# Kernel tuning notes

Measured on AMD Instinct MI355X. Metric: run time of the kernel, lower is better.

The kernel has to match this reference:

```python
import jax, jax.numpy as jnp
import numpy as np

FP4_E2M1_VALUES = jnp.array([0.0, 0.5, 1.0, 1.5, 2.0, 3.0, 4.0, 6.0,
                             -0.0, -0.5, -1.0, -1.5, -2.0, -3.0, -4.0, -6.0],
                            dtype=jnp.float32)

OUT_F, IN_F, BS = 4096, 4096, 16


def setup_inputs() -> dict:
    key = jax.random.key(0)
    k1, k2, k3, k4 = jax.random.split(key, 4)
    x = jax.random.normal(k1, (4, 2048, IN_F), dtype=jnp.float32)
    weight_indices = jax.random.randint(k2, (OUT_F, IN_F // BS, BS), 0, 16, dtype=jnp.int32)
    weight_scales = jax.random.uniform(k3, (OUT_F, IN_F // BS), dtype=jnp.float32)
    bias = jax.random.normal(k4, (OUT_F,), dtype=jnp.float32)
    return {"x": x, "weight_indices": weight_indices,
            "weight_scales": weight_scales, "bias": bias}


def reference(x, weight_indices, weight_scales, bias):
    # Dequantize: gather FP4 values per index, scale per block of 16.
    idx = jnp.clip(weight_indices, 0, 15)              # [O, NB, BS]
    vals = FP4_E2M1_VALUES[idx]                        # [O, NB, BS]
    weight = (vals * weight_scales[:, :, None]).reshape(OUT_F, IN_F)
    # F.linear: y = x @ W^T + b
    return jnp.einsum('bsi,oi->bso', x, weight) + bias
```

## Files before the change

### kernel.cpp

```cpp
#include <hip/hip_runtime.h>
#include <hip/hip_bf16.h>

static constexpr int M_TOT = 8192;
static constexpr int N_TOT = 4096;
static constexpr int K_TOT = 4096;

static constexpr int BM = 256, BN = 256, BK = 32;
static constexpr int NT = K_TOT / BK;
static constexpr int GTHREADS = 512;
static constexpr int BUF_BYTES = 32768;
static constexpr int LDS_BYTES = 4 * BUF_BYTES;

typedef __bf16 bf16x8 __attribute__((ext_vector_type(8)));
typedef float f32x4 __attribute__((ext_vector_type(4)));
typedef unsigned short u16x8 __attribute__((ext_vector_type(8)));

__device__ __forceinline__ unsigned short f2bf(float f) {
  return __builtin_bit_cast(unsigned short, (__bf16)f);
}

__device__ __forceinline__ float fp4_decode(int idx) {
  unsigned u = (unsigned)idx & 15u;
  unsigned sgn = (u >> 3) << 31;
  unsigned mag = u & 7u;
  unsigned e = mag >> 1, m = mag & 1u;
  unsigned bits = (e == 0u) ? (m ? 0x3F000000u : 0u)
                            : (((126u + e) << 23) | (m << 22));
  return __uint_as_float(bits | sgn);
}

__device__ __forceinline__ void glds16(const void* g, void* l) {
  __builtin_amdgcn_global_load_lds(
      (__attribute__((address_space(1))) void*)g,
      (__attribute__((address_space(3))) void*)l, 16, 0, 0);
}

__global__ __launch_bounds__(256) void dequant_w_kernel(
    const int* __restrict__ idx, const float* __restrict__ scales,
    unsigned short* __restrict__ W) {
  const int t = blockIdx.x * 256 + threadIdx.x;
  const int4 v = reinterpret_cast<const int4*>(idx)[t];
  const float s = scales[t >> 2];
  ushort4 o;
  o.x = f2bf(fp4_decode(v.x) * s);
  o.y = f2bf(fp4_decode(v.y) * s);
  o.z = f2bf(fp4_decode(v.z) * s);
  o.w = f2bf(fp4_decode(v.w) * s);
  reinterpret_cast<ushort4*>(W)[t] = o;
}

__global__ __launch_bounds__(256) void convert_x_kernel(
    const float* __restrict__ x, unsigned short* __restrict__ A) {
  const int t = blockIdx.x * 256 + threadIdx.x;
  const float4* xp = reinterpret_cast<const float4*>(x);
  const float4 a = xp[2 * t], b = xp[2 * t + 1];
  u16x8 o;
  o[0] = f2bf(a.x); o[1] = f2bf(a.y); o[2] = f2bf(a.z); o[3] = f2bf(a.w);
  o[4] = f2bf(b.x); o[5] = f2bf(b.y); o[6] = f2bf(b.z); o[7] = f2bf(b.w);
  reinterpret_cast<u16x8*>(A)[t] = o;
}

__global__ __launch_bounds__(GTHREADS, 1) void gemm256(
    const unsigned short* __restrict__ A, const unsigned short* __restrict__ B,
    const float* __restrict__ bias, float* __restrict__ out) {
  extern __shared__ char smem[];

  const int t = threadIdx.x;
  const int lane = t & 63, wid = t >> 6;
  const int wr = wid >> 2;
  const int wc = wid & 3;
  const int ln = lane & 15;
  const int kc = lane >> 4;

  const int bid = blockIdx.x;
  const int bmi = (bid & 7) * 4 + ((bid >> 3) & 3);
  const int bni = bid >> 5;
  const int bm0 = bmi * BM, bn0 = bni * BN;

  const int row_s = t >> 2;
  const int kcd = (t & 3) ^ ((t >> 3) & 3);
  const unsigned short* gA = A + (size_t)(bm0 + row_s) * K_TOT + kcd * 8;
  const unsigned short* gB = B + (size_t)(bn0 + row_s) * K_TOT + kcd * 8;
  char* ldsA = smem + t * 16;
  char* ldsB = smem + 16384 + t * 16;

  const int swz = (kc ^ ((ln >> 1) & 3)) * 16;
  const int base_a = (wr * 128 + ln) * 64 + swz;
  const int base_b = 16384 + (wc * 64 + ln) * 64 + swz;

  f32x4 acc[8][4];
#pragma unroll
  for (int i = 0; i < 8; ++i)
#pragma unroll
    for (int j = 0; j < 4; ++j) acc[i][j] = f32x4{0.f, 0.f, 0.f, 0.f};

  bf16x8 afA[4], afB[4], bfE[4], bfO[4];

#define STAGE_A(kt, bufi) do {                                          \
    const unsigned short* s_ = gA + (size_t)(kt) * BK;                  \
    glds16(s_, ldsA + (bufi) * BUF_BYTES);                              \
    glds16(s_ + (size_t)128 * K_TOT, ldsA + (bufi) * BUF_BYTES + 8192); \
  } while (0)
#define STAGE_B(kt, bufi) do {                                          \
    const unsigned short* s_ = gB + (size_t)(kt) * BK;                  \
    glds16(s_, ldsB + (bufi) * BUF_BYTES);                              \
    glds16(s_ + (size_t)128 * K_TOT, ldsB + (bufi) * BUF_BYTES + 8192); \
  } while (0)

#define READ_AF(dst, bufi, mb) do {                                     \
    const char* p_ = smem + (bufi) * BUF_BYTES + base_a + (mb) * 1024;  \
    dst[0] = *(const bf16x8*)(p_);                                      \
    dst[1] = *(const bf16x8*)(p_ + 1024);                               \
    dst[2] = *(const bf16x8*)(p_ + 2048);                               \
    dst[3] = *(const bf16x8*)(p_ + 3072);                               \
  } while (0)
#define READ_BF(dst, bufi) do {                                         \
    const char* p_ = smem + (bufi) * BUF_BYTES + base_b;                \
    dst[0] = *(const bf16x8*)(p_);                                      \
    dst[1] = *(const bf16x8*)(p_ + 1024);                               \
    dst[2] = *(const bf16x8*)(p_ + 2048);                               \
    dst[3] = *(const bf16x8*)(p_ + 3072);                               \
  } while (0)

#define MFMA16(afs, bfs, mb) do {                                       \
    __builtin_amdgcn_s_setprio(1);                                      \
    _Pragma("unroll")                                                   \
    for (int m_ = 0; m_ < 4; ++m_)                                      \
      _Pragma("unroll")                                                 \
      for (int n_ = 0; n_ < 4; ++n_)                                    \
        acc[(mb) + m_][n_] = __builtin_amdgcn_mfma_f32_16x16x32_bf16(   \
            afs[m_], bfs[n_], acc[(mb) + m_][n_], 0, 0, 0);             \
    __builtin_amdgcn_s_setprio(0);                                      \
  } while (0)

#define VM(n) asm volatile("s_waitcnt vmcnt(" #n ")" ::: "memory")
#define BAR __builtin_amdgcn_s_barrier()

#define PH_A(tt, rb, sb, bfc) do { \
    READ_AF(afB, rb, 4);           \
    STAGE_A((tt) + 3, sb);         \
    MFMA16(afA, bfc, 0);           \
    VM(6); BAR;                    \
  } while (0)
#define PH_B(tt, rbn, sb, bfc, bfn) do { \
    READ_AF(afA, rbn, 0);                \
    READ_BF(bfn, rbn);                   \
    STAGE_B((tt) + 3, sb);               \
    MFMA16(afB, bfc, 4);                 \
    BAR;                                 \
  } while (0)

  STAGE_A(0, 0); STAGE_B(0, 0);
  asm volatile("" ::: "memory");
  STAGE_A(1, 1); STAGE_B(1, 1);
  asm volatile("" ::: "memory");
  STAGE_A(2, 2); STAGE_B(2, 2);
  VM(8);
  BAR;
  READ_AF(afA, 0, 0);
  READ_BF(bfE, 0);

#pragma unroll 1
  for (int tt = 0; tt < NT - 4; tt += 4) {
    PH_A(tt + 0, 0, 3, bfE);
    PH_B(tt + 0, 1, 3, bfE, bfO);
    PH_A(tt + 1, 1, 0, bfO);
    PH_B(tt + 1, 2, 0, bfO, bfE);
    PH_A(tt + 2, 2, 1, bfE);
    PH_B(tt + 2, 3, 1, bfE, bfO);
    PH_A(tt + 3, 3, 2, bfO);
    PH_B(tt + 3, 0, 2, bfO, bfE);
  }

  READ_AF(afB, 0, 4); STAGE_A(127, 3); MFMA16(afA, bfE, 0); VM(6); BAR;
  READ_AF(afA, 1, 0); READ_BF(bfO, 1); STAGE_B(127, 3); MFMA16(afB, bfE, 4); BAR;
  READ_AF(afB, 1, 4); MFMA16(afA, bfO, 0); VM(4); BAR;
  READ_AF(afA, 2, 0); READ_BF(bfE, 2); MFMA16(afB, bfO, 4); BAR;
  READ_AF(afB, 2, 4); MFMA16(afA, bfE, 0); VM(0); BAR;
  READ_AF(afA, 3, 0); READ_BF(bfO, 3); MFMA16(afB, bfE, 4); BAR;
  READ_AF(afB, 3, 4); MFMA16(afA, bfO, 0);
  MFMA16(afB, bfO, 4);

  const int orow0 = bm0 + wr * 128 + (lane >> 4) * 4;
  const int ocol0 = bn0 + wc * 64 + ln;
  float bj[4];
#pragma unroll
  for (int n = 0; n < 4; ++n) bj[n] = bias[ocol0 + n * 16];
#pragma unroll
  for (int mi = 0; mi < 8; ++mi)
#pragma unroll
    for (int n = 0; n < 4; ++n)
#pragma unroll
      for (int q = 0; q < 4; ++q)
        out[(size_t)(orow0 + mi * 16 + q) * N_TOT + ocol0 + n * 16] =
            acc[mi][n][q] + bj[n];
}

extern "C" void kernel_launch(void* const* d_in, const int* in_sizes, int n_in,
                              void* d_out, int out_size, void* d_ws, size_t ws_size,
                              hipStream_t stream) {
  const float* x = (const float*)d_in[0];
  const int* widx = (const int*)d_in[1];
  const float* wsc = (const float*)d_in[2];
  const float* bias = (const float*)d_in[3];
  float* out = (float*)d_out;

  unsigned short* Abf = (unsigned short*)d_ws;
  unsigned short* Wbf = (unsigned short*)((char*)d_ws + (size_t)M_TOT * K_TOT * 2);

  convert_x_kernel<<<dim3((M_TOT * (size_t)K_TOT / 8) / 256), dim3(256), 0, stream>>>(x, Abf);
  dequant_w_kernel<<<dim3((N_TOT * (size_t)K_TOT / 4) / 256), dim3(256), 0, stream>>>(widx, wsc, Wbf);

  (void)hipFuncSetAttribute((const void*)gemm256,
                            hipFuncAttributeMaxDynamicSharedMemorySize, LDS_BYTES);
  gemm256<<<dim3((M_TOT / BM) * (N_TOT / BN)), dim3(GTHREADS), LDS_BYTES, stream>>>(
      Abf, Wbf, bias, out);
}
```

Measured before the change: 279.2 us.

## Switch GEMM inner product to 32x32x16 bf16 MFMA tiles

```diff
diff --git a/kernel.cpp b/kernel.cpp
--- a/kernel.cpp
+++ b/kernel.cpp
@@ -12,7 +12,7 @@
 static constexpr int LDS_BYTES = 4 * BUF_BYTES;
 
 typedef __bf16 bf16x8 __attribute__((ext_vector_type(8)));
-typedef float f32x4 __attribute__((ext_vector_type(4)));
+typedef float f32x16 __attribute__((ext_vector_type(16)));
 typedef unsigned short u16x8 __attribute__((ext_vector_type(8)));
 
 __device__ __forceinline__ unsigned short f2bf(float f) {
@@ -69,8 +69,8 @@
   const int lane = t & 63, wid = t >> 6;
   const int wr = wid >> 2;
   const int wc = wid & 3;
-  const int ln = lane & 15;
-  const int kc = lane >> 4;
+  const int l31 = lane & 31;
+  const int kh = lane >> 5;
 
   const int bid = blockIdx.x;
   const int bmi = (bid & 7) * 4 + ((bid >> 3) & 3);
@@ -84,70 +84,75 @@
   char* ldsA = smem + t * 16;
   char* ldsB = smem + 16384 + t * 16;
 
-  const int swz = (kc ^ ((ln >> 1) & 3)) * 16;
-  const int base_a = (wr * 128 + ln) * 64 + swz;
-  const int base_b = 16384 + (wc * 64 + ln) * 64 + swz;
-
-  f32x4 acc[8][4];
-#pragma unroll
-  for (int i = 0; i < 8; ++i)
-#pragma unroll
-    for (int j = 0; j < 4; ++j) acc[i][j] = f32x4{0.f, 0.f, 0.f, 0.f};
-
-  bf16x8 afA[4], afB[4], bfE[4], bfO[4];
+  const int s_ = (l31 >> 1) & 3;
+  const int c0 = ((0 | kh) ^ s_) * 16;
+  const int c1 = ((2 | kh) ^ s_) * 16;
+  const int a_row = (wr * 128 + l31) * 64;
+  const int b_row = 16384 + (wc * 64 + l31) * 64;
+  const int base_a0 = a_row + c0, base_a1 = a_row + c1;
+  const int base_b0 = b_row + c0, base_b1 = b_row + c1;
+
+  f32x16 acc[4][2];
+#pragma unroll
+  for (int i = 0; i < 4; ++i)
+#pragma unroll
+    for (int j = 0; j < 2; ++j)
+#pragma unroll
+      for (int r = 0; r < 16; ++r) acc[i][j][r] = 0.f;
+
+  bf16x8 afA[4], afB[4], bfA[2], bfB[2];
 
 #define STAGE_A(kt, bufi) do {                                          \
-    const unsigned short* s_ = gA + (size_t)(kt) * BK;                  \
-    glds16(s_, ldsA + (bufi) * BUF_BYTES);                              \
-    glds16(s_ + (size_t)128 * K_TOT, ldsA + (bufi) * BUF_BYTES + 8192); \
+    const unsigned short* p_ = gA + (size_t)(kt) * BK;                  \
+    glds16(p_, ldsA + (bufi) * BUF_BYTES);                              \
+    glds16(p_ + (size_t)128 * K_TOT, ldsA + (bufi) * BUF_BYTES + 8192); \
   } while (0)
 #define STAGE_B(kt, bufi) do {                                          \
-    const unsigned short* s_ = gB + (size_t)(kt) * BK;                  \
-    glds16(s_, ldsB + (bufi) * BUF_BYTES);                              \
-    glds16(s_ + (size_t)128 * K_TOT, ldsB + (bufi) * BUF_BYTES + 8192); \
-  } while (0)
-
-#define READ_AF(dst, bufi, mb) do {                                     \
-    const char* p_ = smem + (bufi) * BUF_BYTES + base_a + (mb) * 1024;  \
+    const unsigned short* p_ = gB + (size_t)(kt) * BK;                  \
+    glds16(p_, ldsB + (bufi) * BUF_BYTES);                              \
+    glds16(p_ + (size_t)128 * K_TOT, ldsB + (bufi) * BUF_BYTES + 8192); \
+  } while (0)
+
+#define READ_A(dst, bufi, ksb) do {                                     \
+    const char* p_ = smem + (bufi) * BUF_BYTES + (ksb);                 \
     dst[0] = *(const bf16x8*)(p_);                                      \
-    dst[1] = *(const bf16x8*)(p_ + 1024);                               \
-    dst[2] = *(const bf16x8*)(p_ + 2048);                               \
-    dst[3] = *(const bf16x8*)(p_ + 3072);                               \
-  } while (0)
-#define READ_BF(dst, bufi) do {                                         \
-    const char* p_ = smem + (bufi) * BUF_BYTES + base_b;                \
+    dst[1] = *(const bf16x8*)(p_ + 2048);                               \
+    dst[2] = *(const bf16x8*)(p_ + 4096);                               \
+    dst[3] = *(const bf16x8*)(p_ + 6144);                               \
+  } while (0)
+#define READ_B(dst, bufi, ksb) do {                                     \
+    const char* p_ = smem + (bufi) * BUF_BYTES + (ksb);                 \
     dst[0] = *(const bf16x8*)(p_);                                      \
-    dst[1] = *(const bf16x8*)(p_ + 1024);                               \
-    dst[2] = *(const bf16x8*)(p_ + 2048);                               \
-    dst[3] = *(const bf16x8*)(p_ + 3072);                               \
-  } while (0)
-
-#define MFMA16(afs, bfs, mb) do {                                       \
+    dst[1] = *(const bf16x8*)(p_ + 2048);                               \
+  } while (0)
+
+#define MFMA8(afs, bfs) do {                                            \
     __builtin_amdgcn_s_setprio(1);                                      \
     _Pragma("unroll")                                                   \
     for (int m_ = 0; m_ < 4; ++m_)                                      \
       _Pragma("unroll")                                                 \
-      for (int n_ = 0; n_ < 4; ++n_)                                    \
-        acc[(mb) + m_][n_] = __builtin_amdgcn_mfma_f32_16x16x32_bf16(   \
-            afs[m_], bfs[n_], acc[(mb) + m_][n_], 0, 0, 0);             \
+      for (int n_ = 0; n_ < 2; ++n_)                                    \
+        acc[m_][n_] = __builtin_amdgcn_mfma_f32_32x32x16_bf16(          \
+            afs[m_], bfs[n_], acc[m_][n_], 0, 0, 0);                    \
     __builtin_amdgcn_s_setprio(0);                                      \
   } while (0)
 
 #define VM(n) asm volatile("s_waitcnt vmcnt(" #n ")" ::: "memory")
 #define BAR __builtin_amdgcn_s_barrier()
 
-#define PH_A(tt, rb, sb, bfc) do { \
-    READ_AF(afB, rb, 4);           \
-    STAGE_A((tt) + 3, sb);         \
-    MFMA16(afA, bfc, 0);           \
-    VM(6); BAR;                    \
-  } while (0)
-#define PH_B(tt, rbn, sb, bfc, bfn) do { \
-    READ_AF(afA, rbn, 0);                \
-    READ_BF(bfn, rbn);                   \
-    STAGE_B((tt) + 3, sb);               \
-    MFMA16(afB, bfc, 4);                 \
-    BAR;                                 \
+#define PH_A(tt, rb, sb) do {                  \
+    READ_A(afB, rb, base_a1);                  \
+    READ_B(bfB, rb, base_b1);                  \
+    STAGE_A((tt) + 3, sb);                     \
+    MFMA8(afA, bfA);                           \
+    VM(6); BAR;                                \
+  } while (0)
+#define PH_B(tt, rbn, sb) do {                 \
+    READ_A(afA, rbn, base_a0);                 \
+    READ_B(bfA, rbn, base_b0);                 \
+    STAGE_B((tt) + 3, sb);                     \
+    MFMA8(afB, bfB);                           \
+    BAR;                                       \
   } while (0)
 
   STAGE_A(0, 0); STAGE_B(0, 0);
@@ -157,43 +162,47 @@
   STAGE_A(2, 2); STAGE_B(2, 2);
   VM(8);
   BAR;
-  READ_AF(afA, 0, 0);
-  READ_BF(bfE, 0);
+  READ_A(afA, 0, base_a0);
+  READ_B(bfA, 0, base_b0);
 
 #pragma unroll 1
   for (int tt = 0; tt < NT - 4; tt += 4) {
-    PH_A(tt + 0, 0, 3, bfE);
-    PH_B(tt + 0, 1, 3, bfE, bfO);
-    PH_A(tt + 1, 1, 0, bfO);
-    PH_B(tt + 1, 2, 0, bfO, bfE);
-    PH_A(tt + 2, 2, 1, bfE);
-    PH_B(tt + 2, 3, 1, bfE, bfO);
-    PH_A(tt + 3, 3, 2, bfO);
-    PH_B(tt + 3, 0, 2, bfO, bfE);
+    PH_A(tt + 0, 0, 3); PH_B(tt + 0, 1, 3);
+    PH_A(tt + 1, 1, 0); PH_B(tt + 1, 2, 0);
+    PH_A(tt + 2, 2, 1); PH_B(tt + 2, 3, 1);
+    PH_A(tt + 3, 3, 2); PH_B(tt + 3, 0, 2);
   }
 
-  READ_AF(afB, 0, 4); STAGE_A(127, 3); MFMA16(afA, bfE, 0); VM(6); BAR;
-  READ_AF(afA, 1, 0); READ_BF(bfO, 1); STAGE_B(127, 3); MFMA16(afB, bfE, 4); BAR;
-  READ_AF(afB, 1, 4); MFMA16(afA, bfO, 0); VM(4); BAR;
-  READ_AF(afA, 2, 0); READ_BF(bfE, 2); MFMA16(afB, bfO, 4); BAR;
-  READ_AF(afB, 2, 4); MFMA16(afA, bfE, 0); VM(0); BAR;
-  READ_AF(afA, 3, 0); READ_BF(bfO, 3); MFMA16(afB, bfE, 4); BAR;
-  READ_AF(afB, 3, 4); MFMA16(afA, bfO, 0);
-  MFMA16(afB, bfO, 4);
-
-  const int orow0 = bm0 + wr * 128 + (lane >> 4) * 4;
-  const int ocol0 = bn0 + wc * 64 + ln;
-  float bj[4];
-#pragma unroll
-  for (int n = 0; n < 4; ++n) bj[n] = bias[ocol0 + n * 16];
-#pragma unroll
-  for (int mi = 0; mi < 8; ++mi)
-#pragma unroll
-    for (int n = 0; n < 4; ++n)
-#pragma unroll
-      for (int q = 0; q < 4; ++q)
-        out[(size_t)(orow0 + mi * 16 + q) * N_TOT + ocol0 + n * 16] =
-            acc[mi][n][q] + bj[n];
+  READ_A(afB, 0, base_a1); READ_B(bfB, 0, base_b1);
+  STAGE_A(127, 3); MFMA8(afA, bfA); VM(6); BAR;
+  READ_A(afA, 1, base_a0); READ_B(bfA, 1, base_b0);
+  STAGE_B(127, 3); MFMA8(afB, bfB); BAR;
+  READ_A(afB, 1, base_a1); READ_B(bfB, 1, base_b1);
+  MFMA8(afA, bfA); VM(4); BAR;
+  READ_A(afA, 2, base_a0); READ_B(bfA, 2, base_b0);
+  MFMA8(afB, bfB); BAR;
+  READ_A(afB, 2, base_a1); READ_B(bfB, 2, base_b1);
+  MFMA8(afA, bfA); VM(0); BAR;
+  READ_A(afA, 3, base_a0); READ_B(bfA, 3, base_b0);
+  MFMA8(afB, bfB); BAR;
+  READ_A(afB, 3, base_a1); READ_B(bfB, 3, base_b1);
+  MFMA8(afA, bfA);
+  MFMA8(afB, bfB);
+
+  const int orow_b = bm0 + wr * 128 + 4 * kh;
+  const int ocol_b = bn0 + wc * 64 + l31;
+  float bj[2];
+  bj[0] = bias[ocol_b];
+  bj[1] = bias[ocol_b + 32];
+#pragma unroll
+  for (int mi = 0; mi < 4; ++mi)
+#pragma unroll
+    for (int ni = 0; ni < 2; ++ni)
+#pragma unroll
+      for (int r = 0; r < 16; ++r) {
+        const int row = orow_b + mi * 32 + (r & 3) + 8 * (r >> 2);
+        out[(size_t)row * N_TOT + ocol_b + ni * 32] = acc[mi][ni][r] + bj[ni];
+      }
 }
 
 extern "C" void kernel_launch(void* const* d_in, const int* in_sizes, int n_in,
```

New measurement: 304.7 us. 9.1% more time.

## Restructure GEMM main loop into two 64-wide K double buffers with eight-phase schedule

Applied to the files above, without the earlier changes.

```diff
diff --git a/kernel.cpp b/kernel.cpp
--- a/kernel.cpp
+++ b/kernel.cpp
@@ -5,11 +5,9 @@
 static constexpr int N_TOT = 4096;
 static constexpr int K_TOT = 4096;
 
-static constexpr int BM = 256, BN = 256, BK = 32;
-static constexpr int NT = K_TOT / BK;
+static constexpr int BM = 256, BN = 256;
 static constexpr int GTHREADS = 512;
-static constexpr int BUF_BYTES = 32768;
-static constexpr int LDS_BYTES = 4 * BUF_BYTES;
+static constexpr int LDS_BYTES = 131072;
 
 typedef __bf16 bf16x8 __attribute__((ext_vector_type(8)));
 typedef float f32x4 __attribute__((ext_vector_type(4)));
@@ -69,8 +67,7 @@
   const int lane = t & 63, wid = t >> 6;
   const int wr = wid >> 2;
   const int wc = wid & 3;
-  const int ln = lane & 15;
-  const int kc = lane >> 4;
+  const int l15 = lane & 15;
 
   const int bid = blockIdx.x;
   const int bmi = (bid & 7) * 4 + ((bid >> 3) & 3);
@@ -79,14 +76,14 @@
 
   const int row_s = t >> 2;
   const int kcd = (t & 3) ^ ((t >> 3) & 3);
-  const unsigned short* gA = A + (size_t)(bm0 + row_s) * K_TOT + kcd * 8;
-  const unsigned short* gB = B + (size_t)(bn0 + row_s) * K_TOT + kcd * 8;
-  char* ldsA = smem + t * 16;
-  char* ldsB = smem + 16384 + t * 16;
-
-  const int swz = (kc ^ ((ln >> 1) & 3)) * 16;
-  const int base_a = (wr * 128 + ln) * 64 + swz;
-  const int base_b = 16384 + (wc * 64 + ln) * 64 + swz;
+  const unsigned short* pA = A + (size_t)(bm0 + row_s) * K_TOT + kcd * 8;
+  const unsigned short* pB = B + (size_t)(bn0 + row_s) * K_TOT + kcd * 8;
+  char* stA = smem + t * 16;
+  char* stB = smem + 32768 + t * 16;
+
+  const int swz = ((lane >> 4) ^ ((l15 >> 1) & 3)) * 16;
+  const int base_a = (wr * 128 + l15) * 64 + swz;
+  const int base_b = 32768 + (wc * 64 + l15) * 64 + swz;
 
   f32x4 acc[8][4];
 #pragma unroll
@@ -94,95 +91,98 @@
 #pragma unroll
     for (int j = 0; j < 4; ++j) acc[i][j] = f32x4{0.f, 0.f, 0.f, 0.f};
 
-  bf16x8 afA[4], afB[4], bfE[4], bfO[4];
-
-#define STAGE_A(kt, bufi) do {                                          \
-    const unsigned short* s_ = gA + (size_t)(kt) * BK;                  \
-    glds16(s_, ldsA + (bufi) * BUF_BYTES);                              \
-    glds16(s_ + (size_t)128 * K_TOT, ldsA + (bufi) * BUF_BYTES + 8192); \
-  } while (0)
-#define STAGE_B(kt, bufi) do {                                          \
-    const unsigned short* s_ = gB + (size_t)(kt) * BK;                  \
-    glds16(s_, ldsB + (bufi) * BUF_BYTES);                              \
-    glds16(s_ + (size_t)128 * K_TOT, ldsB + (bufi) * BUF_BYTES + 8192); \
-  } while (0)
-
-#define READ_AF(dst, bufi, mb) do {                                     \
-    const char* p_ = smem + (bufi) * BUF_BYTES + base_a + (mb) * 1024;  \
-    dst[0] = *(const bf16x8*)(p_);                                      \
-    dst[1] = *(const bf16x8*)(p_ + 1024);                               \
-    dst[2] = *(const bf16x8*)(p_ + 2048);                               \
-    dst[3] = *(const bf16x8*)(p_ + 3072);                               \
-  } while (0)
-#define READ_BF(dst, bufi) do {                                         \
-    const char* p_ = smem + (bufi) * BUF_BYTES + base_b;                \
-    dst[0] = *(const bf16x8*)(p_);                                      \
-    dst[1] = *(const bf16x8*)(p_ + 1024);                               \
-    dst[2] = *(const bf16x8*)(p_ + 2048);                               \
-    dst[3] = *(const bf16x8*)(p_ + 3072);                               \
-  } while (0)
-
-#define MFMA16(afs, bfs, mb) do {                                       \
-    __builtin_amdgcn_s_setprio(1);                                      \
-    _Pragma("unroll")                                                   \
-    for (int m_ = 0; m_ < 4; ++m_)                                      \
-      _Pragma("unroll")                                                 \
-      for (int n_ = 0; n_ < 4; ++n_)                                    \
-        acc[(mb) + m_][n_] = __builtin_amdgcn_mfma_f32_16x16x32_bf16(   \
-            afs[m_], bfs[n_], acc[(mb) + m_][n_], 0, 0, 0);             \
-    __builtin_amdgcn_s_setprio(0);                                      \
+  bf16x8 afQ[4], bfQ[4];
+
+#define STG_A(T, s, doff) do {                                           \
+    const unsigned short* p_ = pA + (T) * 64 + (s) * 32;                 \
+    glds16(p_, stA + (doff) + (s) * 16384);                              \
+    glds16(p_ + (size_t)128 * K_TOT, stA + (doff) + (s) * 16384 + 8192); \
+  } while (0)
+#define STG_B(T, s, doff) do {                                           \
+    const unsigned short* p_ = pB + (T) * 64 + (s) * 32;                 \
+    glds16(p_, stB + (doff) + (s) * 16384);                              \
+    glds16(p_ + (size_t)128 * K_TOT, stB + (doff) + (s) * 16384 + 8192); \
+  } while (0)
+
+#define RD_A4(doff, s, mh) do {                                          \
+    const char* p_ = smem + (doff) + (s) * 16384 + base_a + (mh) * 4096; \
+    afQ[0] = *(const bf16x8*)(p_);                                       \
+    afQ[1] = *(const bf16x8*)(p_ + 1024);                                \
+    afQ[2] = *(const bf16x8*)(p_ + 2048);                                \
+    afQ[3] = *(const bf16x8*)(p_ + 3072);                                \
+  } while (0)
+#define RD_B4(doff, s) do {                                              \
+    const char* p_ = smem + (doff) + (s) * 16384 + base_b;               \
+    bfQ[0] = *(const bf16x8*)(p_);                                       \
+    bfQ[1] = *(const bf16x8*)(p_ + 1024);                                \
+    bfQ[2] = *(const bf16x8*)(p_ + 2048);                                \
+    bfQ[3] = *(const bf16x8*)(p_ + 3072);                                \
+  } while (0)
+
+#define MF16(mb) do {                                                    \
+    __builtin_amdgcn_s_setprio(1);                                       \
+    _Pragma("unroll")                                                    \
+    for (int m_ = 0; m_ < 4; ++m_)                                       \
+      _Pragma("unroll")                                                  \
+      for (int n_ = 0; n_ < 4; ++n_)                                     \
+        acc[(mb) + m_][n_] = __builtin_amdgcn_mfma_f32_16x16x32_bf16(    \
+            afQ[m_], bfQ[n_], acc[(mb) + m_][n_], 0, 0, 0);              \
+    __builtin_amdgcn_s_setprio(0);                                       \
   } while (0)
 
 #define VM(n) asm volatile("s_waitcnt vmcnt(" #n ")" ::: "memory")
 #define BAR __builtin_amdgcn_s_barrier()
 
-#define PH_A(tt, rb, sb, bfc) do { \
-    READ_AF(afB, rb, 4);           \
-    STAGE_A((tt) + 3, sb);         \
-    MFMA16(afA, bfc, 0);           \
-    VM(6); BAR;                    \
-  } while (0)
-#define PH_B(tt, rbn, sb, bfc, bfn) do { \
-    READ_AF(afA, rbn, 0);                \
-    READ_BF(bfn, rbn);                   \
-    STAGE_B((tt) + 3, sb);               \
-    MFMA16(afB, bfc, 4);                 \
-    BAR;                                 \
-  } while (0)
-
-  STAGE_A(0, 0); STAGE_B(0, 0);
-  asm volatile("" ::: "memory");
-  STAGE_A(1, 1); STAGE_B(1, 1);
-  asm volatile("" ::: "memory");
-  STAGE_A(2, 2); STAGE_B(2, 2);
-  VM(8);
+  STG_B(0, 0, 0);
+  STG_A(0, 0, 0);
+  STG_B(0, 1, 0);
+  STG_A(0, 1, 0);
+  STG_B(1, 0, 65536);
+  STG_A(1, 0, 65536);
+  STG_B(1, 1, 65536);
+  VM(10);
   BAR;
-  READ_AF(afA, 0, 0);
-  READ_BF(bfE, 0);
 
 #pragma unroll 1
-  for (int tt = 0; tt < NT - 4; tt += 4) {
-    PH_A(tt + 0, 0, 3, bfE);
-    PH_B(tt + 0, 1, 3, bfE, bfO);
-    PH_A(tt + 1, 1, 0, bfO);
-    PH_B(tt + 1, 2, 0, bfO, bfE);
-    PH_A(tt + 2, 2, 1, bfE);
-    PH_B(tt + 2, 3, 1, bfE, bfO);
-    PH_A(tt + 3, 3, 2, bfO);
-    PH_B(tt + 3, 0, 2, bfO, bfE);
+  for (int i = 0; i < 31; ++i) {
+    const int T = 2 * i, U = 2 * i + 1;
+    RD_A4(0, 0, 0); RD_B4(0, 0); STG_A(U, 1, 65536);
+    BAR; MF16(0); VM(12); BAR;
+    RD_A4(0, 0, 1); STG_B(T + 2, 0, 0);
+    BAR; MF16(4); VM(10); BAR;
+    RD_A4(0, 1, 0); RD_B4(0, 1); STG_A(T + 2, 0, 0);
+    BAR; MF16(0); VM(12); BAR;
+    RD_A4(0, 1, 1); STG_B(T + 2, 1, 0);
+    BAR; MF16(4); VM(10); BAR;
+    RD_A4(65536, 0, 0); RD_B4(65536, 0); STG_A(T + 2, 1, 0);
+    BAR; MF16(0); VM(12); BAR;
+    RD_A4(65536, 0, 1); STG_B(U + 2, 0, 65536);
+    BAR; MF16(4); VM(10); BAR;
+    RD_A4(65536, 1, 0); RD_B4(65536, 1); STG_A(U + 2, 0, 65536);
+    BAR; MF16(0); VM(12); BAR;
+    RD_A4(65536, 1, 1); STG_B(U + 2, 1, 65536);
+    BAR; MF16(4); VM(10); BAR;
   }
 
-  READ_AF(afB, 0, 4); STAGE_A(127, 3); MFMA16(afA, bfE, 0); VM(6); BAR;
-  READ_AF(afA, 1, 0); READ_BF(bfO, 1); STAGE_B(127, 3); MFMA16(afB, bfE, 4); BAR;
-  READ_AF(afB, 1, 4); MFMA16(afA, bfO, 0); VM(4); BAR;
-  READ_AF(afA, 2, 0); READ_BF(bfE, 2); MFMA16(afB, bfO, 4); BAR;
-  READ_AF(afB, 2, 4); MFMA16(afA, bfE, 0); VM(0); BAR;
-  READ_AF(afA, 3, 0); READ_BF(bfO, 3); MFMA16(afB, bfE, 4); BAR;
-  READ_AF(afB, 3, 4); MFMA16(afA, bfO, 0);
-  MFMA16(afB, bfO, 4);
+  RD_A4(0, 0, 0); RD_B4(0, 0); STG_A(63, 1, 65536);
+  BAR; MF16(0); VM(12); BAR;
+  RD_A4(0, 0, 1);
+  BAR; MF16(4); VM(8); BAR;
+  RD_A4(0, 1, 0); RD_B4(0, 1);
+  BAR; MF16(0); VM(8); BAR;
+  RD_A4(0, 1, 1);
+  BAR; MF16(4); VM(4); BAR;
+  RD_A4(65536, 0, 0); RD_B4(65536, 0);
+  BAR; MF16(0); VM(4); BAR;
+  RD_A4(65536, 0, 1);
+  BAR; MF16(4); VM(0); BAR;
+  RD_A4(65536, 1, 0); RD_B4(65536, 1);
+  BAR; MF16(0); BAR;
+  RD_A4(65536, 1, 1);
+  MF16(4);
 
   const int orow0 = bm0 + wr * 128 + (lane >> 4) * 4;
-  const int ocol0 = bn0 + wc * 64 + ln;
+  const int ocol0 = bn0 + wc * 64 + l15;
   float bj[4];
 #pragma unroll
   for (int n = 0; n < 4; ++n) bj[n] = bias[ocol0 + n * 16];
```

Result: no change. 282.2 us (+1.1%).

## Collapse two-phase LDS/MFMA ping-pong into single-phase per K-tile schedule

Applied to the files above, without the earlier changes.

```diff
diff --git a/kernel.cpp b/kernel.cpp
--- a/kernel.cpp
+++ b/kernel.cpp
@@ -94,60 +94,56 @@
 #pragma unroll
     for (int j = 0; j < 4; ++j) acc[i][j] = f32x4{0.f, 0.f, 0.f, 0.f};
 
-  bf16x8 afA[4], afB[4], bfE[4], bfO[4];
+  bf16x8 af[8], bf[4];
 
 #define STAGE_A(kt, bufi) do {                                          \
-    const unsigned short* s_ = gA + (size_t)(kt) * BK;                  \
-    glds16(s_, ldsA + (bufi) * BUF_BYTES);                              \
-    glds16(s_ + (size_t)128 * K_TOT, ldsA + (bufi) * BUF_BYTES + 8192); \
+    const unsigned short* p_ = gA + (size_t)(kt) * BK;                  \
+    glds16(p_, ldsA + (bufi) * BUF_BYTES);                              \
+    glds16(p_ + (size_t)128 * K_TOT, ldsA + (bufi) * BUF_BYTES + 8192); \
   } while (0)
 #define STAGE_B(kt, bufi) do {                                          \
-    const unsigned short* s_ = gB + (size_t)(kt) * BK;                  \
-    glds16(s_, ldsB + (bufi) * BUF_BYTES);                              \
-    glds16(s_ + (size_t)128 * K_TOT, ldsB + (bufi) * BUF_BYTES + 8192); \
-  } while (0)
-
-#define READ_AF(dst, bufi, mb) do {                                     \
-    const char* p_ = smem + (bufi) * BUF_BYTES + base_a + (mb) * 1024;  \
-    dst[0] = *(const bf16x8*)(p_);                                      \
-    dst[1] = *(const bf16x8*)(p_ + 1024);                               \
-    dst[2] = *(const bf16x8*)(p_ + 2048);                               \
-    dst[3] = *(const bf16x8*)(p_ + 3072);                               \
-  } while (0)
-#define READ_BF(dst, bufi) do {                                         \
-    const char* p_ = smem + (bufi) * BUF_BYTES + base_b;                \
-    dst[0] = *(const bf16x8*)(p_);                                      \
-    dst[1] = *(const bf16x8*)(p_ + 1024);                               \
-    dst[2] = *(const bf16x8*)(p_ + 2048);                               \
-    dst[3] = *(const bf16x8*)(p_ + 3072);                               \
-  } while (0)
-
-#define MFMA16(afs, bfs, mb) do {                                       \
+    const unsigned short* p_ = gB + (size_t)(kt) * BK;                  \
+    glds16(p_, ldsB + (bufi) * BUF_BYTES);                              \
+    glds16(p_ + (size_t)128 * K_TOT, ldsB + (bufi) * BUF_BYTES + 8192); \
+  } while (0)
+
+#define RD_ALL(bufi) do {                                               \
+    const char* pa_ = smem + (bufi) * BUF_BYTES + base_a;               \
+    const char* pb_ = smem + (bufi) * BUF_BYTES + base_b;               \
+    af[0] = *(const bf16x8*)(pa_);                                      \
+    af[1] = *(const bf16x8*)(pa_ + 1024);                               \
+    af[2] = *(const bf16x8*)(pa_ + 2048);                               \
+    af[3] = *(const bf16x8*)(pa_ + 3072);                               \
+    bf[0] = *(const bf16x8*)(pb_);                                      \
+    bf[1] = *(const bf16x8*)(pb_ + 1024);                               \
+    bf[2] = *(const bf16x8*)(pb_ + 2048);                               \
+    bf[3] = *(const bf16x8*)(pb_ + 3072);                               \
+    af[4] = *(const bf16x8*)(pa_ + 4096);                               \
+    af[5] = *(const bf16x8*)(pa_ + 5120);                               \
+    af[6] = *(const bf16x8*)(pa_ + 6144);                               \
+    af[7] = *(const bf16x8*)(pa_ + 7168);                               \
+  } while (0)
+
+#define MF32() do {                                                     \
     __builtin_amdgcn_s_setprio(1);                                      \
     _Pragma("unroll")                                                   \
-    for (int m_ = 0; m_ < 4; ++m_)                                      \
+    for (int m_ = 0; m_ < 8; ++m_)                                      \
       _Pragma("unroll")                                                 \
       for (int n_ = 0; n_ < 4; ++n_)                                    \
-        acc[(mb) + m_][n_] = __builtin_amdgcn_mfma_f32_16x16x32_bf16(   \
-            afs[m_], bfs[n_], acc[(mb) + m_][n_], 0, 0, 0);             \
+        acc[m_][n_] = __builtin_amdgcn_mfma_f32_16x16x32_bf16(          \
+            af[m_], bf[n_], acc[m_][n_], 0, 0, 0);                      \
     __builtin_amdgcn_s_setprio(0);                                      \
   } while (0)
 
 #define VM(n) asm volatile("s_waitcnt vmcnt(" #n ")" ::: "memory")
 #define BAR __builtin_amdgcn_s_barrier()
 
-#define PH_A(tt, rb, sb, bfc) do { \
-    READ_AF(afB, rb, 4);           \
-    STAGE_A((tt) + 3, sb);         \
-    MFMA16(afA, bfc, 0);           \
-    VM(6); BAR;                    \
-  } while (0)
-#define PH_B(tt, rbn, sb, bfc, bfn) do { \
-    READ_AF(afA, rbn, 0);                \
-    READ_BF(bfn, rbn);                   \
-    STAGE_B((tt) + 3, sb);               \
-    MFMA16(afB, bfc, 4);                 \
-    BAR;                                 \
+#define PH(tt, cb, sb) do { \
+    STAGE_A((tt) + 3, sb);  \
+    STAGE_B((tt) + 3, sb);  \
+    RD_ALL(cb);             \
+    MF32();                 \
+    VM(8); BAR;             \
   } while (0)
 
   STAGE_A(0, 0); STAGE_B(0, 0);
@@ -157,29 +153,19 @@
   STAGE_A(2, 2); STAGE_B(2, 2);
   VM(8);
   BAR;
-  READ_AF(afA, 0, 0);
-  READ_BF(bfE, 0);
 
 #pragma unroll 1
   for (int tt = 0; tt < NT - 4; tt += 4) {
-    PH_A(tt + 0, 0, 3, bfE);
-    PH_B(tt + 0, 1, 3, bfE, bfO);
-    PH_A(tt + 1, 1, 0, bfO);
-    PH_B(tt + 1, 2, 0, bfO, bfE);
-    PH_A(tt + 2, 2, 1, bfE);
-    PH_B(tt + 2, 3, 1, bfE, bfO);
-    PH_A(tt + 3, 3, 2, bfO);
-    PH_B(tt + 3, 0, 2, bfO, bfE);
+    PH(tt + 0, 0, 3);
+    PH(tt + 1, 1, 0);
+    PH(tt + 2, 2, 1);
+    PH(tt + 3, 3, 2);
   }
 
-  READ_AF(afB, 0, 4); STAGE_A(127, 3); MFMA16(afA, bfE, 0); VM(6); BAR;
-  READ_AF(afA, 1, 0); READ_BF(bfO, 1); STAGE_B(127, 3); MFMA16(afB, bfE, 4); BAR;
-  READ_AF(afB, 1, 4); MFMA16(afA, bfO, 0); VM(4); BAR;
-  READ_AF(afA, 2, 0); READ_BF(bfE, 2); MFMA16(afB, bfO, 4); BAR;
-  READ_AF(afB, 2, 4); MFMA16(afA, bfE, 0); VM(0); BAR;
-  READ_AF(afA, 3, 0); READ_BF(bfO, 3); MFMA16(afB, bfE, 4); BAR;
-  READ_AF(afB, 3, 4); MFMA16(afA, bfO, 0);
-  MFMA16(afB, bfO, 4);
+  PH(124, 0, 3);
+  RD_ALL(1); MF32(); VM(4); BAR;
+  RD_ALL(2); MF32(); VM(0); BAR;
+  RD_ALL(3); MF32();
 
   const int orow0 = bm0 + wr * 128 + (lane >> 4) * 4;
   const int ocol0 = bn0 + wc * 64 + ln;
```

After: 283.7 us. No clear change (+1.6%).
